# Optimization experiments

Measured on AMD Instinct MI355X. Metric: run time of the kernel, lower is better.

## Reference

```python
import math
import jax, jax.numpy as jnp
import numpy as np

B, S, IN_DIM = 4, 2048, 256
L, H, NHEAD, FFN = 3, 256, 4, 1024
CF, CB = 32, 32  # context_forward / context_backward window
EPS = 1e-5


def sinusoidal_pe(seq_len, d_model):
    pos = jnp.arange(seq_len, dtype=jnp.float32)[:, None]
    div = jnp.exp(jnp.arange(0, d_model, 2, dtype=jnp.float32) * (-math.log(10000.0) / d_model))
    pe = jnp.zeros((seq_len, d_model), dtype=jnp.float32)
    pe = pe.at[:, 0::2].set(jnp.sin(pos * div))
    pe = pe.at[:, 1::2].set(jnp.cos(pos * div))
    return pe


def band_mask(s):
    # True = allowed: -CB <= j - i <= CF (sliding window, from triu/transpose construction)
    i = jnp.arange(s)[:, None]
    j = jnp.arange(s)[None, :]
    return (j - i <= CF) & (i - j <= CB)


def layer_norm(x, g, b):
    mu = jnp.mean(x, axis=-1, keepdims=True)
    var = jnp.mean((x - mu) ** 2, axis=-1, keepdims=True)
    return (x - mu) * jax.lax.rsqrt(var + EPS) * g + b


def mha(x, wqkv, bqkv, wo, bo, mask):
    b, s, d = x.shape
    dh = d // NHEAD
    qkv = x @ wqkv.T + bqkv  # [b, s, 3d]
    q, k, v = jnp.split(qkv, 3, axis=-1)
    split = lambda t: t.reshape(b, s, NHEAD, dh).transpose(0, 2, 1, 3)  # [b, h, s, dh]
    q, k, v = split(q), split(k), split(v)
    scores = jnp.einsum('bhqd,bhkd->bhqk', q, k) / math.sqrt(dh)
    scores = jnp.where(mask, scores, -jnp.inf)
    attn = jax.nn.softmax(scores, axis=-1)
    o = jnp.einsum('bhqk,bhkd->bhqd', attn, v).transpose(0, 2, 1, 3).reshape(b, s, d)
    return o @ wo.T + bo


def setup_inputs() -> dict:
    key = jax.random.key(0)
    ks = jax.random.split(key, 12)
    sc = 0.02
    inp = {
        'x': jax.random.normal(ks[0], (B, S, IN_DIM), dtype=jnp.float32),
        'w_in': sc * jax.random.normal(ks[1], (H, IN_DIM), dtype=jnp.float32),
        'w_out': sc * jax.random.normal(ks[2], (IN_DIM, H), dtype=jnp.float32),
        'b_out': jnp.zeros((IN_DIM,), dtype=jnp.float32),
        'qkv_w': sc * jax.random.normal(ks[3], (L, 3 * H, H), dtype=jnp.float32),
        'qkv_b': jnp.zeros((L, 3 * H), dtype=jnp.float32),
        'out_w': sc * jax.random.normal(ks[4], (L, H, H), dtype=jnp.float32),
        'out_b': jnp.zeros((L, H), dtype=jnp.float32),
        'ln1_g': jnp.ones((L, H), dtype=jnp.float32),
        'ln1_b': jnp.zeros((L, H), dtype=jnp.float32),
        'ln2_g': jnp.ones((L, H), dtype=jnp.float32),
        'ln2_b': jnp.zeros((L, H), dtype=jnp.float32),
        'ff1_w': sc * jax.random.normal(ks[5], (L, FFN, H), dtype=jnp.float32),
        'ff1_b': jnp.zeros((L, FFN), dtype=jnp.float32),
        'ff2_w': sc * jax.random.normal(ks[6], (L, H, FFN), dtype=jnp.float32),
        'ff2_b': jnp.zeros((L, H), dtype=jnp.float32),
        'lnf_g': jnp.ones((H,), dtype=jnp.float32),
        'lnf_b': jnp.zeros((H,), dtype=jnp.float32),
    }
    return inp


def reference(x, w_in, w_out, b_out, qkv_w, qkv_b, out_w, out_b,
              ln1_g, ln1_b, ln2_g, ln2_b, ff1_w, ff1_b, ff2_w, ff2_b,
              lnf_g, lnf_b):
    b, s, _ = x.shape
    mask = band_mask(s)
    h = math.sqrt(H) * (x @ w_in.T) + sinusoidal_pe(s, H)[None]
    for l in range(L):  # pre-norm transformer encoder layers (relu FFN, eval/no-dropout)
        h = h + mha(layer_norm(h, ln1_g[l], ln1_b[l]), qkv_w[l], qkv_b[l], out_w[l], out_b[l], mask)
        z = layer_norm(h, ln2_g[l], ln2_b[l])
        h = h + (jax.nn.relu(z @ ff1_w[l].T + ff1_b[l]) @ ff2_w[l].T + ff2_b[l])
    h = layer_norm(h, lnf_g, lnf_b)
    return h @ w_out.T + b_out
```

## Files before the change

kernel.cpp:

```cpp
#include <hip/hip_runtime.h>
#include <hip/hip_bf16.h>
#include <math.h>

#define SEQ 2048
#define BATCH 4
#define HDIM 256
#define NHEAD 4
#define FFN_DIM 1024
#define MTOT (BATCH*SEQ)

typedef __attribute__((ext_vector_type(8))) short bf16x8;
typedef __attribute__((ext_vector_type(4))) float f32x4;

__device__ __forceinline__ bf16x8 cvt8(const float* p)
{
    float4 a = *(const float4*)p;
    float4 b = *(const float4*)(p + 4);
    union { bf16x8 v; __hip_bfloat16 e[8]; } u;
    u.e[0] = __float2bfloat16(a.x); u.e[1] = __float2bfloat16(a.y);
    u.e[2] = __float2bfloat16(a.z); u.e[3] = __float2bfloat16(a.w);
    u.e[4] = __float2bfloat16(b.x); u.e[5] = __float2bfloat16(b.y);
    u.e[6] = __float2bfloat16(b.z); u.e[7] = __float2bfloat16(b.w);
    return u.v;
}

__global__ __launch_bounds__(256)
void cvt_all(const float* __restrict__ w_in, const float* __restrict__ w_out,
             const float* __restrict__ qkv_w, const float* __restrict__ out_w,
             const float* __restrict__ ff1_w, const float* __restrict__ ff2_w,
             __hip_bfloat16* __restrict__ wb)
{
    int i = blockIdx.x * 256 + threadIdx.x;
    size_t e = (size_t)i * 8;

    const float* srcbase; size_t rbase; int kshift;
    if (e < 720896) {
        if (e < 65536)       { srcbase = w_in;  rbase = 0;      kshift = 8; }
        else if (e < 131072) { srcbase = w_out; rbase = 65536;  kshift = 8; }
        else                 { srcbase = qkv_w; rbase = 131072; kshift = 8; }
    } else if (e < 917504)   { srcbase = out_w; rbase = 720896; kshift = 8; }
    else if (e < 1703936)    { srcbase = ff1_w; rbase = 917504; kshift = 8; }
    else                     { srcbase = ff2_w; rbase = 1703936; kshift = 10; }

    size_t local = e - rbase;
    int K = 1 << kshift;
    int row = (int)(local >> kshift);
    int k   = (int)(local & (K - 1));

    size_t dst = rbase
               + ((size_t)(row >> 4) * (K >> 5) + (k >> 5)) * 512
               + (size_t)((((k >> 3) & 3) << 4) | (row & 15)) * 8;

    *(bf16x8*)(wb + dst) = cvt8(srcbase + local);
}

__device__ __forceinline__ bf16x8 fragW(const short* W, int n0, int k0, int K, int lane)
{
    return *(const bf16x8*)(W + ((size_t)(n0 >> 4) * (K >> 5) + (k0 >> 5)) * 512 + lane * 8);
}

__global__ __launch_bounds__(256)
void embed_pe(const float* __restrict__ X, const __hip_bfloat16* __restrict__ W,
              float* __restrict__ hbuf)
{
    int tid = threadIdx.x, wave = tid >> 6, lane = tid & 63;
    int wm = wave >> 1, wn = wave & 1;
    int rowBase = blockIdx.y * 64 + wm * 32;
    int colBase = blockIdx.x * 64 + wn * 32;
    int lr = lane & 15, hi = lane >> 4;

    const float* px0 = X + (size_t)(rowBase + lr) * HDIM + hi * 8;
    const float* px1 = px0 + (size_t)16 * HDIM;
    const short* Wb  = (const short*)W;

    f32x4 acc[2][2];
    acc[0][0] = (f32x4){0.f,0.f,0.f,0.f}; acc[0][1] = (f32x4){0.f,0.f,0.f,0.f};
    acc[1][0] = (f32x4){0.f,0.f,0.f,0.f}; acc[1][1] = (f32x4){0.f,0.f,0.f,0.f};

    #pragma unroll
    for (int k0 = 0; k0 < 256; k0 += 32) {
        bf16x8 a0 = cvt8(px0 + k0);
        bf16x8 a1 = cvt8(px1 + k0);
        bf16x8 b0 = fragW(Wb, colBase,      k0, 256, lane);
        bf16x8 b1 = fragW(Wb, colBase + 16, k0, 256, lane);
        acc[0][0] = __builtin_amdgcn_mfma_f32_16x16x32_bf16(a0, b0, acc[0][0], 0,0,0);
        acc[0][1] = __builtin_amdgcn_mfma_f32_16x16x32_bf16(a0, b1, acc[0][1], 0,0,0);
        acc[1][0] = __builtin_amdgcn_mfma_f32_16x16x32_bf16(a1, b0, acc[1][0], 0,0,0);
        acc[1][1] = __builtin_amdgcn_mfma_f32_16x16x32_bf16(a1, b1, acc[1][1], 0,0,0);
    }

    int cc = lane & 15, quad = lane >> 4;
    #pragma unroll
    for (int mt = 0; mt < 2; mt++)
        #pragma unroll
        for (int nt = 0; nt < 2; nt++) {
            int col = colBase + nt*16 + cc;
            int i2 = col & ~1;
            float freq = __expf((float)i2 * (-9.210340371976184f / 256.0f));
            #pragma unroll
            for (int r = 0; r < 4; r++) {
                int row = rowBase + mt*16 + quad*4 + r;
                float arg = (float)(row & (SEQ-1)) * freq;
                float pe = (col & 1) ? __cosf(arg) : __sinf(arg);
                hbuf[(size_t)row*HDIM + col] = 16.0f*acc[mt][nt][r] + pe;
            }
        }
}

template<int MODE, int NT>
__global__ __launch_bounds__(256)
void gemm_ln(const float* __restrict__ h,
             const float* __restrict__ g, const float* __restrict__ bln,
             const __hip_bfloat16* __restrict__ W,
             const float* __restrict__ bias,
             __hip_bfloat16* __restrict__ obf, float* __restrict__ of32,
             int N, int ldw)
{
    constexpr int NTW = NT / 32;
    __shared__ __align__(16) short A_lds[64][264];

    int tid = threadIdx.x, wave = tid >> 6, lane = tid & 63;
    int wm = wave >> 1, wn = wave & 1;
    int rowBase = blockIdx.y * 64;
    int colBase = blockIdx.x * NT + wn * (NT / 2);

    {
        float4 gv = *(const float4*)(g + lane * 4);
        float4 bv = *(const float4*)(bln + lane * 4);
        #pragma unroll
        for (int rr = 0; rr < 16; rr += 4) {
            float4 xv[4];
            #pragma unroll
            for (int u = 0; u < 4; u++)
                xv[u] = *(const float4*)(h + (size_t)(rowBase + wave*16 + rr + u)*HDIM + lane*4);
            #pragma unroll
            for (int u = 0; u < 4; u++) {
                float s = xv[u].x + xv[u].y + xv[u].z + xv[u].w;
                #pragma unroll
                for (int off = 32; off >= 1; off >>= 1) s += __shfl_xor(s, off);
                float mu = s * (1.0f/256.0f);
                float d0 = xv[u].x-mu, d1 = xv[u].y-mu, d2 = xv[u].z-mu, d3 = xv[u].w-mu;
                float v = d0*d0 + d1*d1 + d2*d2 + d3*d3;
                #pragma unroll
                for (int off = 32; off >= 1; off >>= 1) v += __shfl_xor(v, off);
                float rstd = rsqrtf(v * (1.0f/256.0f) + 1e-5f);
                union { short e[4]; uint2 w2; } o;
                o.e[0] = (short)__bfloat16_as_ushort(__float2bfloat16(d0*rstd*gv.x + bv.x));
                o.e[1] = (short)__bfloat16_as_ushort(__float2bfloat16(d1*rstd*gv.y + bv.y));
                o.e[2] = (short)__bfloat16_as_ushort(__float2bfloat16(d2*rstd*gv.z + bv.z));
                o.e[3] = (short)__bfloat16_as_ushort(__float2bfloat16(d3*rstd*gv.w + bv.w));
                *(uint2*)&A_lds[wave*16 + rr + u][lane*4] = o.w2;
            }
        }
    }
    __syncthreads();

    int lr = lane & 15, hi = lane >> 4;
    f32x4 acc[2][NTW];
    #pragma unroll
    for (int mt = 0; mt < 2; mt++)
        #pragma unroll
        for (int nt = 0; nt < NTW; nt++)
            acc[mt][nt] = (f32x4){0.f,0.f,0.f,0.f};

    const short* Ws = (const short*)W;
    #pragma unroll
    for (int k0 = 0; k0 < 256; k0 += 32) {
        bf16x8 af[2], bfr[NTW];
        #pragma unroll
        for (int mt = 0; mt < 2; mt++)
            af[mt] = *(const bf16x8*)&A_lds[wm*32 + mt*16 + lr][k0 + hi*8];
        #pragma unroll
        for (int nt = 0; nt < NTW; nt++)
            bfr[nt] = fragW(Ws, colBase + nt*16, k0, 256, lane);
        #pragma unroll
        for (int mt = 0; mt < 2; mt++)
            #pragma unroll
            for (int nt = 0; nt < NTW; nt++)
                acc[mt][nt] = __builtin_amdgcn_mfma_f32_16x16x32_bf16(af[mt], bfr[nt], acc[mt][nt], 0,0,0);
    }

    int cc = lane & 15, quad = lane >> 4;
    #pragma unroll
    for (int mt = 0; mt < 2; mt++)
        #pragma unroll
        for (int nt = 0; nt < NTW; nt++) {
            int col = colBase + nt*16 + cc;
            float bv = bias[col];
            #pragma unroll
            for (int r = 0; r < 4; r++) {
                int row = rowBase + wm*32 + mt*16 + quad*4 + r;
                float c = acc[mt][nt][r] + bv;
                if (MODE == 4) { of32[(size_t)row*N + col] = c; }
                else {
                    int sec = col >> 8, hd = (col >> 6) & 3, d = col & 63;
                    int srow = row & (SEQ - 1);
                    size_t base = (size_t)sec * 2097152
                                + (size_t)(((row >> 11) << 2) | hd) * 131072;
                    size_t idx;
                    if (sec < 2)
                        idx = base + (size_t)(srow >> 4) * 1024 + (size_t)(d >> 5) * 512
                            + (size_t)((((d >> 3) & 3) << 4) | (srow & 15)) * 8 + (d & 7);
                    else
                        idx = base + (size_t)srow * 64 + d;
                    obf[idx] = __float2bfloat16(c);
                }
            }
        }
}

struct AttnLDS {
    __align__(16) __hip_bfloat16 Vt[64][128];
    __align__(16) __hip_bfloat16 Pl[32][96];
    float sm[2][32], ss[2][32];
};

template<int LAST>
__global__ __launch_bounds__(1024)
void attn_ffn(const __hip_bfloat16* __restrict__ qkvd,
              const __hip_bfloat16* __restrict__ ow,
              const float* __restrict__ ob,
              float* __restrict__ h,
              const float* __restrict__ g, const float* __restrict__ bln,
              const __hip_bfloat16* __restrict__ W1, const float* __restrict__ b1,
              const __hip_bfloat16* __restrict__ W2, const float* __restrict__ b2,
              const float* __restrict__ gf, const float* __restrict__ bf,
              const __hip_bfloat16* __restrict__ Wout, const float* __restrict__ bout,
              float* __restrict__ outp)
{
    __shared__ union SMem {
        AttnLDS asl[4];
        struct {
            __align__(16) short A[32][264];
            __align__(16) short Z[2][32][264];
        } f;
    } U;
    __shared__ __align__(16) short att_lds[32][264];
    __shared__ __align__(16) float H_lds[32][260];

    int tid  = threadIdx.x;
    int wave = tid >> 6, lane = tid & 63;
    int grp  = wave >> 2, w4 = wave & 3, ltid = tid & 255;
    int b    = blockIdx.y, i0 = blockIdx.x * 32;
    int klo  = i0 - 32;

    int lr = lane & 15, hi = lane >> 4;
    int cc = lane & 15, quad = lane >> 4;

    int hd = grp;
    AttnLDS& S = U.asl[grp];
    const short* Qd = (const short*)qkvd + (size_t)(b * 4 + hd) * 131072;
    const short* Kd = Qd + 2097152;
    const short* Vd = Qd + 4194304;
    int qh = w4 & 1, seg = w4 >> 1;
    int qoff = qh * 16 + quad * 4;

    int vm = ltid & 7, vrl = ltid >> 3, vdp = vm * 8;
    bf16x8 vr[3];
    #pragma unroll
    for (int rr = 0; rr < 3; rr++) {
        int j = klo + rr * 32 + vrl;
        j = j < 0 ? 0 : (j > SEQ - 1 ? SEQ - 1 : j);
        vr[rr] = *(const bf16x8*)(Vd + (size_t)j * 64 + vdp);
    }
    bf16x8 qf[2];
    #pragma unroll
    for (int ds = 0; ds < 2; ds++)
        qf[ds] = *(const bf16x8*)(Qd + (size_t)((i0 >> 4) + qh) * 1024 + ds * 512 + lane * 8);
    bf16x8 kf[3][2];
    #pragma unroll
    for (int t = 0; t < 3; t++) {
        int jt = (klo + seg * 48 + t * 16) >> 4;
        jt = jt < 0 ? 0 : (jt > 127 ? 127 : jt);
        kf[t][0] = *(const bf16x8*)(Kd + (size_t)jt * 1024 + lane * 8);
        kf[t][1] = *(const bf16x8*)(Kd + (size_t)jt * 1024 + 512 + lane * 8);
    }
    float hold[2][4];
    {
        const float* hp = h + (size_t)(b * SEQ + i0) * HDIM + wave * 16 + cc;
        #pragma unroll
        for (int mt = 0; mt < 2; mt++)
            #pragma unroll
            for (int r = 0; r < 4; r++)
                hold[mt][r] = hp[(size_t)(mt*16 + quad*4 + r) * HDIM];
    }

    {
        union { bf16x8 v; short e[8]; } u;
        #pragma unroll
        for (int rr = 0; rr < 3; rr++) {
            int row = rr * 32 + vrl;
            int colp = row ^ (vm << 3);
            u.v = vr[rr];
            #pragma unroll
            for (int jj = 0; jj < 8; jj++)
                *(short*)&S.Vt[vdp + jj][colp] = u.e[jj];
        }
    }

    f32x4 sacc[3];
    #pragma unroll
    for (int t = 0; t < 3; t++) {
        f32x4 a = (f32x4){0.f,0.f,0.f,0.f};
        a = __builtin_amdgcn_mfma_f32_16x16x32_bf16(qf[0], kf[t][0], a, 0,0,0);
        a = __builtin_amdgcn_mfma_f32_16x16x32_bf16(qf[1], kf[t][1], a, 0,0,0);
        sacc[t] = a;
    }

    float s[3][4];
    #pragma unroll
    for (int t = 0; t < 3; t++) {
        int koff = seg * 48 + t * 16 + cc;
        int jj = klo + koff;
        #pragma unroll
        for (int r = 0; r < 4; r++) {
            int rel = koff - (qoff + r);
            bool ok = (jj >= 0) && (jj < SEQ) && (rel >= 0) && (rel <= 64);
            s[t][r] = ok ? sacc[t][r] * 0.125f : -1e30f;
        }
    }

    float mrow[4], srow[4];
    #pragma unroll
    for (int r = 0; r < 4; r++)
        mrow[r] = fmaxf(fmaxf(s[0][r], s[1][r]), s[2][r]);
    #pragma unroll
    for (int off = 8; off >= 1; off >>= 1)
        #pragma unroll
        for (int r = 0; r < 4; r++)
            mrow[r] = fmaxf(mrow[r], __shfl_xor(mrow[r], off));
    #pragma unroll
    for (int r = 0; r < 4; r++)
        srow[r] = __expf(s[0][r]-mrow[r]) + __expf(s[1][r]-mrow[r]) + __expf(s[2][r]-mrow[r]);
    #pragma unroll
    for (int off = 8; off >= 1; off >>= 1)
        #pragma unroll
        for (int r = 0; r < 4; r++)
            srow[r] += __shfl_xor(srow[r], off);
    if (cc == 0) {
        #pragma unroll
        for (int r = 0; r < 4; r++) { S.sm[seg][qoff+r] = mrow[r]; S.ss[seg][qoff+r] = srow[r]; }
    }
    __syncthreads();

    float Mr[4], inv[4];
    #pragma unroll
    for (int r = 0; r < 4; r++) {
        float m0 = S.sm[0][qoff+r], m1 = S.sm[1][qoff+r];
        float M = fmaxf(m0, m1);
        float dn = S.ss[0][qoff+r] * __expf(m0 - M) + S.ss[1][qoff+r] * __expf(m1 - M);
        Mr[r] = M; inv[r] = 1.0f / dn;
    }
    #pragma unroll
    for (int t = 0; t < 3; t++)
        #pragma unroll
        for (int r = 0; r < 4; r++)
            S.Pl[qoff+r][seg*48 + t*16 + cc] = __float2bfloat16(__expf(s[t][r]-Mr[r]) * inv[r]);
    __syncthreads();

    bf16x8 owf[8];
    {
        const short* op = (const short*)ow + (size_t)wave * 8 * 512 + lane * 8;
        #pragma unroll
        for (int i = 0; i < 8; i++)
            owf[i] = *(const bf16x8*)(op + i * 512);
    }

    {
        f32x4 oacc[2];
        oacc[0] = (f32x4){0.f,0.f,0.f,0.f}; oacc[1] = (f32x4){0.f,0.f,0.f,0.f};
        #pragma unroll
        for (int ks = 0; ks < 3; ks++) {
            int kk = ks * 32;
            bf16x8 pf = *(const bf16x8*)&S.Pl[qh*16 + lr][kk + hi*8];
            #pragma unroll
            for (int dt = 0; dt < 2; dt++) {
                int d = seg*32 + dt*16 + lr;
                int colb = (kk + hi*8) ^ (((d >> 3) & 7) << 3);
                bf16x8 vf = *(const bf16x8*)&S.Vt[d][colb];
                oacc[dt] = __builtin_amdgcn_mfma_f32_16x16x32_bf16(pf, vf, oacc[dt], 0,0,0);
            }
        }
        #pragma unroll
        for (int dt = 0; dt < 2; dt++) {
            int col = hd*64 + seg*32 + dt*16 + cc;
            #pragma unroll
            for (int r = 0; r < 4; r++)
                att_lds[qoff + r][col] =
                    (short)__bfloat16_as_ushort(__float2bfloat16(oacc[dt][r]));
        }
    }
    __syncthreads();

    {
        f32x4 acc[2];
        acc[0] = (f32x4){0.f,0.f,0.f,0.f}; acc[1] = (f32x4){0.f,0.f,0.f,0.f};
        #pragma unroll
        for (int i = 0; i < 8; i++) {
            bf16x8 a0 = *(const bf16x8*)&att_lds[lr][i*32 + hi*8];
            bf16x8 a1 = *(const bf16x8*)&att_lds[16 + lr][i*32 + hi*8];
            acc[0] = __builtin_amdgcn_mfma_f32_16x16x32_bf16(a0, owf[i], acc[0], 0,0,0);
            acc[1] = __builtin_amdgcn_mfma_f32_16x16x32_bf16(a1, owf[i], acc[1], 0,0,0);
        }
        float bv = ob[wave*16 + cc];
        #pragma unroll
        for (int mt = 0; mt < 2; mt++)
            #pragma unroll
            for (int r = 0; r < 4; r++)
                H_lds[mt*16 + quad*4 + r][wave*16 + cc] = hold[mt][r] + acc[mt][r] + bv;
    }

    const short* W1s = (const short*)W1;
    const short* W2s = (const short*)W2;
    bf16x8 w1f[8];
    {
        const short* wp = W1s + (size_t)wave * 8 * 512 + lane * 8;
        #pragma unroll
        for (int i = 0; i < 8; i++)
            w1f[i] = *(const bf16x8*)(wp + i * 512);
    }
    __syncthreads();

    {
        float4 gv = *(const float4*)(g + lane * 4);
        float4 bv = *(const float4*)(bln + lane * 4);
        #pragma unroll
        for (int u = 0; u < 2; u++) {
            float4 xv = *(const float4*)&H_lds[wave*2 + u][lane*4];
            float ss2 = xv.x + xv.y + xv.z + xv.w;
            #pragma unroll
            for (int off = 32; off >= 1; off >>= 1) ss2 += __shfl_xor(ss2, off);
            float mu = ss2 * (1.0f/256.0f);
            float d0 = xv.x-mu, d1 = xv.y-mu, d2 = xv.z-mu, d3 = xv.w-mu;
            float v = d0*d0 + d1*d1 + d2*d2 + d3*d3;
            #pragma unroll
            for (int off = 32; off >= 1; off >>= 1) v += __shfl_xor(v, off);
            float rstd = rsqrtf(v * (1.0f/256.0f) + 1e-5f);
            union { short e[4]; uint2 w2; } o;
            o.e[0] = (short)__bfloat16_as_ushort(__float2bfloat16(d0*rstd*gv.x + bv.x));
            o.e[1] = (short)__bfloat16_as_ushort(__float2bfloat16(d1*rstd*gv.y + bv.y));
            o.e[2] = (short)__bfloat16_as_ushort(__float2bfloat16(d2*rstd*gv.z + bv.z));
            o.e[3] = (short)__bfloat16_as_ushort(__float2bfloat16(d3*rstd*gv.w + bv.w));
            *(uint2*)&U.f.A[wave*2 + u][lane*4] = o.w2;
        }
    }
    __syncthreads();

    f32x4 acc2[2];
    acc2[0] = (f32x4){0.f,0.f,0.f,0.f}; acc2[1] = (f32x4){0.f,0.f,0.f,0.f};

    #pragma unroll 1
    for (int kk = 0; kk < 4; kk++) {
        bf16x8 w2f[8];
        {
            const short* wp = W2s + (size_t)(wave * 32 + kk * 8) * 512 + lane * 8;
            #pragma unroll
            for (int i = 0; i < 8; i++)
                w2f[i] = *(const bf16x8*)(wp + i * 512);
        }

        f32x4 acc1[2];
        acc1[0] = (f32x4){0.f,0.f,0.f,0.f}; acc1[1] = (f32x4){0.f,0.f,0.f,0.f};
        #pragma unroll
        for (int i = 0; i < 8; i++) {
            bf16x8 af0 = *(const bf16x8*)&U.f.A[lr][i*32 + hi*8];
            bf16x8 af1 = *(const bf16x8*)&U.f.A[16 + lr][i*32 + hi*8];
            acc1[0] = __builtin_amdgcn_mfma_f32_16x16x32_bf16(af0, w1f[i], acc1[0], 0,0,0);
            acc1[1] = __builtin_amdgcn_mfma_f32_16x16x32_bf16(af1, w1f[i], acc1[1], 0,0,0);
        }

        {
            int col = wave*16 + cc;
            float bb = b1[kk*256 + col];
            #pragma unroll
            for (int mt = 0; mt < 2; mt++)
                #pragma unroll
                for (int r = 0; r < 4; r++) {
                    float z = fmaxf(acc1[mt][r] + bb, 0.f);
                    U.f.Z[kk & 1][mt*16 + quad*4 + r][col] =
                        (short)__bfloat16_as_ushort(__float2bfloat16(z));
                }
        }
        __syncthreads();

        {
            int nk = (kk < 3) ? kk + 1 : 3;
            const short* wp = W1s + (size_t)(nk * 16 + wave) * 8 * 512 + lane * 8;
            #pragma unroll
            for (int i = 0; i < 8; i++)
                w1f[i] = *(const bf16x8*)(wp + i * 512);
        }

        #pragma unroll
        for (int i = 0; i < 8; i++) {
            bf16x8 zf0 = *(const bf16x8*)&U.f.Z[kk & 1][lr][i*32 + hi*8];
            bf16x8 zf1 = *(const bf16x8*)&U.f.Z[kk & 1][16 + lr][i*32 + hi*8];
            acc2[0] = __builtin_amdgcn_mfma_f32_16x16x32_bf16(zf0, w2f[i], acc2[0], 0,0,0);
            acc2[1] = __builtin_amdgcn_mfma_f32_16x16x32_bf16(zf1, w2f[i], acc2[1], 0,0,0);
        }
    }

    if (!LAST) {
        int col = wave*16 + cc;
        float bb = b2[col];
        #pragma unroll
        for (int mt = 0; mt < 2; mt++)
            #pragma unroll
            for (int r = 0; r < 4; r++) {
                int rowl = mt*16 + quad*4 + r;
                int row = b * SEQ + i0 + rowl;
                h[(size_t)row * HDIM + col] = H_lds[rowl][col] + acc2[mt][r] + bb;
            }
    } else {
        {
            int col = wave*16 + cc;
            float bb = b2[col];
            #pragma unroll
            for (int mt = 0; mt < 2; mt++)
                #pragma unroll
                for (int r = 0; r < 4; r++) {
                    int rowl = mt*16 + quad*4 + r;
                    H_lds[rowl][col] = H_lds[rowl][col] + acc2[mt][r] + bb;
                }
        }
        __syncthreads();

        {
            float4 gv = *(const float4*)(gf + lane * 4);
            float4 bv = *(const float4*)(bf + lane * 4);
            #pragma unroll
            for (int u = 0; u < 2; u++) {
                float4 xv = *(const float4*)&H_lds[wave*2 + u][lane*4];
                float ss2 = xv.x + xv.y + xv.z + xv.w;
                #pragma unroll
                for (int off = 32; off >= 1; off >>= 1) ss2 += __shfl_xor(ss2, off);
                float mu = ss2 * (1.0f/256.0f);
                float d0 = xv.x-mu, d1 = xv.y-mu, d2 = xv.z-mu, d3 = xv.w-mu;
                float v = d0*d0 + d1*d1 + d2*d2 + d3*d3;
                #pragma unroll
                for (int off = 32; off >= 1; off >>= 1) v += __shfl_xor(v, off);
                float rstd = rsqrtf(v * (1.0f/256.0f) + 1e-5f);
                union { short e[4]; uint2 w2; } o;
                o.e[0] = (short)__bfloat16_as_ushort(__float2bfloat16(d0*rstd*gv.x + bv.x));
                o.e[1] = (short)__bfloat16_as_ushort(__float2bfloat16(d1*rstd*gv.y + bv.y));
                o.e[2] = (short)__bfloat16_as_ushort(__float2bfloat16(d2*rstd*gv.z + bv.z));
                o.e[3] = (short)__bfloat16_as_ushort(__float2bfloat16(d3*rstd*gv.w + bv.w));
                *(uint2*)&U.f.A[wave*2 + u][lane*4] = o.w2;
            }
        }
        __syncthreads();

        {
            bf16x8 wf[8];
            const short* wp = (const short*)Wout + (size_t)wave * 8 * 512 + lane * 8;
            #pragma unroll
            for (int i = 0; i < 8; i++)
                wf[i] = *(const bf16x8*)(wp + i * 512);

            f32x4 oa[2];
            oa[0] = (f32x4){0.f,0.f,0.f,0.f}; oa[1] = (f32x4){0.f,0.f,0.f,0.f};
            #pragma unroll
            for (int i = 0; i < 8; i++) {
                bf16x8 a0 = *(const bf16x8*)&U.f.A[lr][i*32 + hi*8];
                bf16x8 a1 = *(const bf16x8*)&U.f.A[16 + lr][i*32 + hi*8];
                oa[0] = __builtin_amdgcn_mfma_f32_16x16x32_bf16(a0, wf[i], oa[0], 0,0,0);
                oa[1] = __builtin_amdgcn_mfma_f32_16x16x32_bf16(a1, wf[i], oa[1], 0,0,0);
            }
            int col = wave*16 + cc;
            float bb = bout[col];
            #pragma unroll
            for (int mt = 0; mt < 2; mt++)
                #pragma unroll
                for (int r = 0; r < 4; r++) {
                    int row = b * SEQ + i0 + mt*16 + quad*4 + r;
                    outp[(size_t)row * HDIM + col] = oa[mt][r] + bb;
                }
        }
    }
}

extern "C" void kernel_launch(void* const* d_in, const int* in_sizes, int n_in,
                              void* d_out, int out_size, void* d_ws, size_t ws_size,
                              hipStream_t stream)
{
    const float* x     = (const float*)d_in[0];
    const float* w_in  = (const float*)d_in[1];
    const float* w_out = (const float*)d_in[2];
    const float* b_out = (const float*)d_in[3];
    const float* qkv_w = (const float*)d_in[4];
    const float* qkv_b = (const float*)d_in[5];
    const float* out_w = (const float*)d_in[6];
    const float* out_b = (const float*)d_in[7];
    const float* ln1_g = (const float*)d_in[8];
    const float* ln1_b = (const float*)d_in[9];
    const float* ln2_g = (const float*)d_in[10];
    const float* ln2_b = (const float*)d_in[11];
    const float* ff1_w = (const float*)d_in[12];
    const float* ff1_b = (const float*)d_in[13];
    const float* ff2_w = (const float*)d_in[14];
    const float* ff2_b = (const float*)d_in[15];
    const float* lnf_g = (const float*)d_in[16];
    const float* lnf_b = (const float*)d_in[17];

    char* ws = (char*)d_ws;
    float*          h    = (float*)ws;
    __hip_bfloat16* qkvd = (__hip_bfloat16*)(ws + 8388608);
    __hip_bfloat16* wb   = (__hip_bfloat16*)(ws + 25165824);

    __hip_bfloat16* w_in_b  = wb;
    __hip_bfloat16* w_out_b = wb + 65536;
    __hip_bfloat16* qkv_w_b = wb + 131072;
    __hip_bfloat16* out_w_b = wb + 720896;
    __hip_bfloat16* ff1_w_b = wb + 917504;
    __hip_bfloat16* ff2_w_b = wb + 1703936;

    dim3 blk(256);

    cvt_all<<<1216, blk, 0, stream>>>(w_in, w_out, qkv_w, out_w, ff1_w, ff2_w, wb);

    embed_pe<<<dim3(4, 128), blk, 0, stream>>>(x, w_in_b, h);

    for (int l = 0; l < 3; l++) {
        gemm_ln<5, 128><<<dim3(6, 128), blk, 0, stream>>>(
            h, ln1_g + l*HDIM, ln1_b + l*HDIM,
            qkv_w_b + (size_t)l*768*HDIM, qkv_b + l*768, qkvd, nullptr, 768, HDIM);
        if (l < 2)
            attn_ffn<0><<<dim3(SEQ/32, BATCH), dim3(1024), 0, stream>>>(
                qkvd, out_w_b + (size_t)l*HDIM*HDIM, out_b + l*HDIM, h,
                ln2_g + l*HDIM, ln2_b + l*HDIM,
                ff1_w_b + (size_t)l*FFN_DIM*HDIM, ff1_b + l*FFN_DIM,
                ff2_w_b + (size_t)l*HDIM*FFN_DIM, ff2_b + l*HDIM,
                nullptr, nullptr, nullptr, nullptr, nullptr);
        else
            attn_ffn<1><<<dim3(SEQ/32, BATCH), dim3(1024), 0, stream>>>(
                qkvd, out_w_b + (size_t)l*HDIM*HDIM, out_b + l*HDIM, h,
                ln2_g + l*HDIM, ln2_b + l*HDIM,
                ff1_w_b + (size_t)l*FFN_DIM*HDIM, ff1_b + l*FFN_DIM,
                ff2_w_b + (size_t)l*HDIM*FFN_DIM, ff2_b + l*HDIM,
                lnf_g, lnf_b, w_out_b, b_out, (float*)d_out);
    }
}
```

Measured before the change: 233.8 us.

## Fuse next layer's LN1 and QKV projection into attention-FFN kernel tail

Each attention+FFN block now ends by applying the next layer's LayerNorm and QKV projection on its 32-row tile and writes the QKV output directly. The separate gemm_ln launches for layers 1 and 2, and their re-read of h, go away. QKV buffers are double-buffered (qkvd0/qkvd1) because neighbouring blocks still read the previous layer's K/V inside their attention windows. The price is extra MFMA work and weight loads in the already large 1024-thread kernel, which may add register and occupancy pressure.

Result: faster. 224.1 us (-4.1%).

```diff
diff --git a/kernel.cpp b/kernel.cpp
--- a/kernel.cpp
+++ b/kernel.cpp
@@ -57,6 +57,18 @@
 __device__ __forceinline__ bf16x8 fragW(const short* W, int n0, int k0, int K, int lane)
 {
     return *(const bf16x8*)(W + ((size_t)(n0 >> 4) * (K >> 5) + (k0 >> 5)) * 512 + lane * 8);
+}
+
+__device__ __forceinline__ size_t qkv_idx(int row, int col)
+{
+    int sec = col >> 8, hd = (col >> 6) & 3, d = col & 63;
+    int srow = row & (SEQ - 1);
+    size_t base = (size_t)sec * 2097152
+                + (size_t)(((row >> 11) << 2) | hd) * 131072;
+    if (sec < 2)
+        return base + (size_t)(srow >> 4) * 1024 + (size_t)(d >> 5) * 512
+             + (size_t)((((d >> 3) & 3) << 4) | (srow & 15)) * 8 + (d & 7);
+    return base + (size_t)srow * 64 + d;
 }
 
 __global__ __launch_bounds__(256)
@@ -107,14 +119,13 @@
         }
 }
 
-template<int MODE, int NT>
+template<int NT>
 __global__ __launch_bounds__(256)
 void gemm_ln(const float* __restrict__ h,
              const float* __restrict__ g, const float* __restrict__ bln,
              const __hip_bfloat16* __restrict__ W,
              const float* __restrict__ bias,
-             __hip_bfloat16* __restrict__ obf, float* __restrict__ of32,
-             int N, int ldw)
+             __hip_bfloat16* __restrict__ obf)
 {
     constexpr int NTW = NT / 32;
     __shared__ __align__(16) short A_lds[64][264];
@@ -191,20 +202,7 @@
             for (int r = 0; r < 4; r++) {
                 int row = rowBase + wm*32 + mt*16 + quad*4 + r;
                 float c = acc[mt][nt][r] + bv;
-                if (MODE == 4) { of32[(size_t)row*N + col] = c; }
-                else {
-                    int sec = col >> 8, hd = (col >> 6) & 3, d = col & 63;
-                    int srow = row & (SEQ - 1);
-                    size_t base = (size_t)sec * 2097152
-                                + (size_t)(((row >> 11) << 2) | hd) * 131072;
-                    size_t idx;
-                    if (sec < 2)
-                        idx = base + (size_t)(srow >> 4) * 1024 + (size_t)(d >> 5) * 512
-                            + (size_t)((((d >> 3) & 3) << 4) | (srow & 15)) * 8 + (d & 7);
-                    else
-                        idx = base + (size_t)srow * 64 + d;
-                    obf[idx] = __float2bfloat16(c);
-                }
+                obf[qkv_idx(row, col)] = __float2bfloat16(c);
             }
         }
 }
@@ -215,7 +213,7 @@
     float sm[2][32], ss[2][32];
 };
 
-template<int LAST>
+template<int TAIL>
 __global__ __launch_bounds__(1024)
 void attn_ffn(const __hip_bfloat16* __restrict__ qkvd,
               const __hip_bfloat16* __restrict__ ow,
@@ -224,9 +222,9 @@
               const float* __restrict__ g, const float* __restrict__ bln,
               const __hip_bfloat16* __restrict__ W1, const float* __restrict__ b1,
               const __hip_bfloat16* __restrict__ W2, const float* __restrict__ b2,
-              const float* __restrict__ gf, const float* __restrict__ bf,
-              const __hip_bfloat16* __restrict__ Wout, const float* __restrict__ bout,
-              float* __restrict__ outp)
+              const float* __restrict__ gt, const float* __restrict__ bt,
+              const __hip_bfloat16* __restrict__ Wt, const float* __restrict__ btb,
+              float* __restrict__ outp, __hip_bfloat16* __restrict__ qkv_out)
 {
     __shared__ union SMem {
         AttnLDS asl[4];
@@ -500,7 +498,7 @@
         }
     }
 
-    if (!LAST) {
+    {
         int col = wave*16 + cc;
         float bb = b2[col];
         #pragma unroll
@@ -508,72 +506,97 @@
             #pragma unroll
             for (int r = 0; r < 4; r++) {
                 int rowl = mt*16 + quad*4 + r;
-                int row = b * SEQ + i0 + rowl;
-                h[(size_t)row * HDIM + col] = H_lds[rowl][col] + acc2[mt][r] + bb;
+                float v = H_lds[rowl][col] + acc2[mt][r] + bb;
+                H_lds[rowl][col] = v;
+                if (TAIL == 1) {
+                    int row = b * SEQ + i0 + rowl;
+                    h[(size_t)row * HDIM + col] = v;
+                }
+            }
+    }
+    __syncthreads();
+
+    {
+        float4 gv = *(const float4*)(gt + lane * 4);
+        float4 bv = *(const float4*)(bt + lane * 4);
+        #pragma unroll
+        for (int u = 0; u < 2; u++) {
+            float4 xv = *(const float4*)&H_lds[wave*2 + u][lane*4];
+            float ss2 = xv.x + xv.y + xv.z + xv.w;
+            #pragma unroll
+            for (int off = 32; off >= 1; off >>= 1) ss2 += __shfl_xor(ss2, off);
+            float mu = ss2 * (1.0f/256.0f);
+            float d0 = xv.x-mu, d1 = xv.y-mu, d2 = xv.z-mu, d3 = xv.w-mu;
+            float v = d0*d0 + d1*d1 + d2*d2 + d3*d3;
+            #pragma unroll
+            for (int off = 32; off >= 1; off >>= 1) v += __shfl_xor(v, off);
+            float rstd = rsqrtf(v * (1.0f/256.0f) + 1e-5f);
+            union { short e[4]; uint2 w2; } o;
+            o.e[0] = (short)__bfloat16_as_ushort(__float2bfloat16(d0*rstd*gv.x + bv.x));
+            o.e[1] = (short)__bfloat16_as_ushort(__float2bfloat16(d1*rstd*gv.y + bv.y));
+            o.e[2] = (short)__bfloat16_as_ushort(__float2bfloat16(d2*rstd*gv.z + bv.z));
+            o.e[3] = (short)__bfloat16_as_ushort(__float2bfloat16(d3*rstd*gv.w + bv.w));
+            *(uint2*)&U.f.A[wave*2 + u][lane*4] = o.w2;
+        }
+    }
+    __syncthreads();
+
+    if (TAIL == 2) {
+        bf16x8 wf[8];
+        const short* wp = (const short*)Wt + (size_t)wave * 8 * 512 + lane * 8;
+        #pragma unroll
+        for (int i = 0; i < 8; i++)
+            wf[i] = *(const bf16x8*)(wp + i * 512);
+
+        f32x4 oa[2];
+        oa[0] = (f32x4){0.f,0.f,0.f,0.f}; oa[1] = (f32x4){0.f,0.f,0.f,0.f};
+        #pragma unroll
+        for (int i = 0; i < 8; i++) {
+            bf16x8 a0 = *(const bf16x8*)&U.f.A[lr][i*32 + hi*8];
+            bf16x8 a1 = *(const bf16x8*)&U.f.A[16 + lr][i*32 + hi*8];
+            oa[0] = __builtin_amdgcn_mfma_f32_16x16x32_bf16(a0, wf[i], oa[0], 0,0,0);
+            oa[1] = __builtin_amdgcn_mfma_f32_16x16x32_bf16(a1, wf[i], oa[1], 0,0,0);
+        }
+        int col = wave*16 + cc;
+        float bb = btb[col];
+        #pragma unroll
+        for (int mt = 0; mt < 2; mt++)
+            #pragma unroll
+            for (int r = 0; r < 4; r++) {
+                int row = b * SEQ + i0 + mt*16 + quad*4 + r;
+                outp[(size_t)row * HDIM + col] = oa[mt][r] + bb;
             }
     } else {
-        {
-            int col = wave*16 + cc;
-            float bb = b2[col];
-            #pragma unroll
-            for (int mt = 0; mt < 2; mt++)
-                #pragma unroll
-                for (int r = 0; r < 4; r++) {
-                    int rowl = mt*16 + quad*4 + r;
-                    H_lds[rowl][col] = H_lds[rowl][col] + acc2[mt][r] + bb;
-                }
-        }
-        __syncthreads();
-
-        {
-            float4 gv = *(const float4*)(gf + lane * 4);
-            float4 bv = *(const float4*)(bf + lane * 4);
-            #pragma unroll
-            for (int u = 0; u < 2; u++) {
-                float4 xv = *(const float4*)&H_lds[wave*2 + u][lane*4];
-                float ss2 = xv.x + xv.y + xv.z + xv.w;
-                #pragma unroll
-                for (int off = 32; off >= 1; off >>= 1) ss2 += __shfl_xor(ss2, off);
-                float mu = ss2 * (1.0f/256.0f);
-                float d0 = xv.x-mu, d1 = xv.y-mu, d2 = xv.z-mu, d3 = xv.w-mu;
-                float v = d0*d0 + d1*d1 + d2*d2 + d3*d3;
-                #pragma unroll
-                for (int off = 32; off >= 1; off >>= 1) v += __shfl_xor(v, off);
-                float rstd = rsqrtf(v * (1.0f/256.0f) + 1e-5f);
-                union { short e[4]; uint2 w2; } o;
-                o.e[0] = (short)__bfloat16_as_ushort(__float2bfloat16(d0*rstd*gv.x + bv.x));
-                o.e[1] = (short)__bfloat16_as_ushort(__float2bfloat16(d1*rstd*gv.y + bv.y));
-                o.e[2] = (short)__bfloat16_as_ushort(__float2bfloat16(d2*rstd*gv.z + bv.z));
-                o.e[3] = (short)__bfloat16_as_ushort(__float2bfloat16(d3*rstd*gv.w + bv.w));
-                *(uint2*)&U.f.A[wave*2 + u][lane*4] = o.w2;
+        const short* Wts = (const short*)Wt;
+        f32x4 qa[2][3];
+        #pragma unroll
+        for (int mt = 0; mt < 2; mt++)
+            #pragma unroll
+            for (int nt = 0; nt < 3; nt++)
+                qa[mt][nt] = (f32x4){0.f,0.f,0.f,0.f};
+
+        #pragma unroll
+        for (int k0 = 0; k0 < 256; k0 += 32) {
+            bf16x8 a0 = *(const bf16x8*)&U.f.A[lr][k0 + hi*8];
+            bf16x8 a1 = *(const bf16x8*)&U.f.A[16 + lr][k0 + hi*8];
+            #pragma unroll
+            for (int nt = 0; nt < 3; nt++) {
+                bf16x8 wf = fragW(Wts, wave*48 + nt*16, k0, 256, lane);
+                qa[0][nt] = __builtin_amdgcn_mfma_f32_16x16x32_bf16(a0, wf, qa[0][nt], 0,0,0);
+                qa[1][nt] = __builtin_amdgcn_mfma_f32_16x16x32_bf16(a1, wf, qa[1][nt], 0,0,0);
             }
         }
-        __syncthreads();
-
-        {
-            bf16x8 wf[8];
-            const short* wp = (const short*)Wout + (size_t)wave * 8 * 512 + lane * 8;
-            #pragma unroll
-            for (int i = 0; i < 8; i++)
-                wf[i] = *(const bf16x8*)(wp + i * 512);
-
-            f32x4 oa[2];
-            oa[0] = (f32x4){0.f,0.f,0.f,0.f}; oa[1] = (f32x4){0.f,0.f,0.f,0.f};
-            #pragma unroll
-            for (int i = 0; i < 8; i++) {
-                bf16x8 a0 = *(const bf16x8*)&U.f.A[lr][i*32 + hi*8];
-                bf16x8 a1 = *(const bf16x8*)&U.f.A[16 + lr][i*32 + hi*8];
-                oa[0] = __builtin_amdgcn_mfma_f32_16x16x32_bf16(a0, wf[i], oa[0], 0,0,0);
-                oa[1] = __builtin_amdgcn_mfma_f32_16x16x32_bf16(a1, wf[i], oa[1], 0,0,0);
-            }
-            int col = wave*16 + cc;
-            float bb = bout[col];
+        #pragma unroll
+        for (int nt = 0; nt < 3; nt++) {
+            int col = wave*48 + nt*16 + cc;
+            float bv = btb[col];
             #pragma unroll
             for (int mt = 0; mt < 2; mt++)
                 #pragma unroll
                 for (int r = 0; r < 4; r++) {
                     int row = b * SEQ + i0 + mt*16 + quad*4 + r;
-                    outp[(size_t)row * HDIM + col] = oa[mt][r] + bb;
+                    float c = qa[mt][nt][r] + bv;
+                    qkv_out[qkv_idx(row, col)] = __float2bfloat16(c);
                 }
         }
     }
@@ -603,9 +626,10 @@
     const float* lnf_b = (const float*)d_in[17];
 
     char* ws = (char*)d_ws;
-    float*          h    = (float*)ws;
-    __hip_bfloat16* qkvd = (__hip_bfloat16*)(ws + 8388608);
-    __hip_bfloat16* wb   = (__hip_bfloat16*)(ws + 25165824);
+    float*          h     = (float*)ws;
+    __hip_bfloat16* qkvd0 = (__hip_bfloat16*)(ws + 8388608);
+    __hip_bfloat16* qkvd1 = (__hip_bfloat16*)(ws + 20971520);
+    __hip_bfloat16* wb    = (__hip_bfloat16*)(ws + 33554432);
 
     __hip_bfloat16* w_in_b  = wb;
     __hip_bfloat16* w_out_b = wb + 65536;
@@ -620,23 +644,27 @@
 
     embed_pe<<<dim3(4, 128), blk, 0, stream>>>(x, w_in_b, h);
 
-    for (int l = 0; l < 3; l++) {
-        gemm_ln<5, 128><<<dim3(6, 128), blk, 0, stream>>>(
-            h, ln1_g + l*HDIM, ln1_b + l*HDIM,
-            qkv_w_b + (size_t)l*768*HDIM, qkv_b + l*768, qkvd, nullptr, 768, HDIM);
-        if (l < 2)
-            attn_ffn<0><<<dim3(SEQ/32, BATCH), dim3(1024), 0, stream>>>(
-                qkvd, out_w_b + (size_t)l*HDIM*HDIM, out_b + l*HDIM, h,
-                ln2_g + l*HDIM, ln2_b + l*HDIM,
-                ff1_w_b + (size_t)l*FFN_DIM*HDIM, ff1_b + l*FFN_DIM,
-                ff2_w_b + (size_t)l*HDIM*FFN_DIM, ff2_b + l*HDIM,
-                nullptr, nullptr, nullptr, nullptr, nullptr);
-        else
-            attn_ffn<1><<<dim3(SEQ/32, BATCH), dim3(1024), 0, stream>>>(
-                qkvd, out_w_b + (size_t)l*HDIM*HDIM, out_b + l*HDIM, h,
-                ln2_g + l*HDIM, ln2_b + l*HDIM,
-                ff1_w_b + (size_t)l*FFN_DIM*HDIM, ff1_b + l*FFN_DIM,
-                ff2_w_b + (size_t)l*HDIM*FFN_DIM, ff2_b + l*HDIM,
-                lnf_g, lnf_b, w_out_b, b_out, (float*)d_out);
-    }
-}
+    gemm_ln<128><<<dim3(6, 128), blk, 0, stream>>>(
+        h, ln1_g, ln1_b, qkv_w_b, qkv_b, qkvd0);
+
+    attn_ffn<1><<<dim3(SEQ/32, BATCH), dim3(1024), 0, stream>>>(
+        qkvd0, out_w_b, out_b, h,
+        ln2_g, ln2_b, ff1_w_b, ff1_b, ff2_w_b, ff2_b,
+        ln1_g + HDIM, ln1_b + HDIM,
+        qkv_w_b + (size_t)768*HDIM, qkv_b + 768, nullptr, qkvd1);
+
+    attn_ffn<1><<<dim3(SEQ/32, BATCH), dim3(1024), 0, stream>>>(
+        qkvd1, out_w_b + (size_t)HDIM*HDIM, out_b + HDIM, h,
+        ln2_g + HDIM, ln2_b + HDIM,
+        ff1_w_b + (size_t)FFN_DIM*HDIM, ff1_b + FFN_DIM,
+        ff2_w_b + (size_t)HDIM*FFN_DIM, ff2_b + HDIM,
+        ln1_g + 2*HDIM, ln1_b + 2*HDIM,
+        qkv_w_b + (size_t)2*768*HDIM, qkv_b + 2*768, nullptr, qkvd0);
+
+    attn_ffn<2><<<dim3(SEQ/32, BATCH), dim3(1024), 0, stream>>>(
+        qkvd0, out_w_b + (size_t)2*HDIM*HDIM, out_b + 2*HDIM, h,
+        ln2_g + 2*HDIM, ln2_b + 2*HDIM,
+        ff1_w_b + (size_t)2*FFN_DIM*HDIM, ff1_b + 2*FFN_DIM,
+        ff2_w_b + (size_t)2*HDIM*FFN_DIM, ff2_b + 2*HDIM,
+        lnf_g, lnf_b, w_out_b, b_out, (float*)d_out, nullptr);
+}
```
